# Kernel tuning notes

Hardware: AMD Instinct MI355X
Metric: run time of the kernel (lower is better)

Reference implementation:

```python
import jax, jax.numpy as jnp
import numpy as np

NUM_EMB = 10_000_000
EMB_DIM = 3
B = 16384
HIST = 50
K = 128


def setup_inputs() -> dict:
    key = jax.random.key(0)
    k1, k2, k3, k4, k5, k6, k7, k8, k9 = jax.random.split(key, 9)
    eb_input = jax.random.randint(k1, (B * HIST,), 0, NUM_EMB, dtype=jnp.int64)
    eb_offset = (jnp.arange(B, dtype=jnp.int64) * HIST)  # bag starts
    mlp_input = jax.random.normal(k2, (B, K), dtype=jnp.float32)
    # learned params
    emb_weight = jax.random.normal(k3, (NUM_EMB, EMB_DIM), dtype=jnp.float32)
    w0 = jax.random.normal(k4, (12, K), dtype=jnp.float32) * (1.0 / np.sqrt(K))
    b0 = jax.random.normal(k5, (12,), dtype=jnp.float32) * 0.01
    w1 = jax.random.normal(k6, (6, 12), dtype=jnp.float32) * (1.0 / np.sqrt(12))
    b1 = jax.random.normal(k7, (6,), dtype=jnp.float32) * 0.01
    w2 = jax.random.normal(k8, (3, 6), dtype=jnp.float32) * (1.0 / np.sqrt(6))
    b2 = jax.random.normal(k9, (3,), dtype=jnp.float32) * 0.01
    return {"eb_input": eb_input, "eb_offset": eb_offset, "mlp_input": mlp_input,
            "emb_weight": emb_weight, "w0": w0, "b0": b0, "w1": w1, "b1": b1,
            "w2": w2, "b2": b2}


def _embedding_bag_mean(weight, indices, offsets, num_bags):
    # bag id for each index position (offsets are sorted bag starts, offsets[0]=0)
    n = indices.shape[0]
    seg = jnp.searchsorted(offsets, jnp.arange(n, dtype=offsets.dtype), side='right') - 1
    rows = weight[indices]                                   # [N, 3] gather
    sums = jax.ops.segment_sum(rows, seg, num_segments=num_bags)          # [B, 3]
    cnts = jax.ops.segment_sum(jnp.ones((n,), weight.dtype), seg, num_segments=num_bags)
    return sums / jnp.maximum(cnts, 1.0)[:, None]            # mean mode; empty bag -> 0


def reference(eb_input, eb_offset, mlp_input, emb_weight, w0, b0, w1, b1, w2, b2):
    # All 3 EmbeddingBags alias the SAME module (python list * 3), so one lookup suffices.
    eb_out = _embedding_bag_mean(emb_weight, eb_input, eb_offset, mlp_input.shape[0])
    h = mlp_input @ w0.T + b0
    h = h @ w1.T + b1
    mlp_out = h @ w2.T + b2                                   # [B, 3]
    return jnp.concatenate([eb_out, eb_out, eb_out, mlp_out], axis=1)  # [B, 12]
```

## Files before the change

kernel.cpp:

```cpp
#include <hip/hip_runtime.h>


#define KDIM 128

__global__ __launch_bounds__(KDIM) void collapse_weights_kernel(
    const float* __restrict__ w0, const float* __restrict__ b0,
    const float* __restrict__ w1, const float* __restrict__ b1,
    const float* __restrict__ w2, const float* __restrict__ b2,
    float* __restrict__ ws)
{
    __shared__ float t[6][KDIM];
    __shared__ float tb[6];

    const int k = threadIdx.x;
    for (int i = 0; i < 6; ++i) {
        float acc = 0.f;
        for (int j = 0; j < 12; ++j)
            acc += w1[i * 12 + j] * w0[j * KDIM + k];
        t[i][k] = acc;
    }
    if (k < 6) {
        float acc = 0.f;
        for (int j = 0; j < 12; ++j)
            acc += w1[k * 12 + j] * b0[j];
        tb[k] = acc + b1[k];
    }
    __syncthreads();

    for (int o = 0; o < 3; ++o) {
        float acc = 0.f;
        for (int i = 0; i < 6; ++i)
            acc += w2[o * 6 + i] * t[i][k];
        ws[o * KDIM + k] = acc;
    }
    if (k == 0) {
        for (int o = 0; o < 3; ++o) {
            float acc = 0.f;
            for (int i = 0; i < 6; ++i)
                acc += w2[o * 6 + i] * tb[i];
            ws[3 * KDIM + o] = acc + b2[o];
        }
    }
}

__global__ __launch_bounds__(256) void fused_embbag_mlp_kernel(
    const int* __restrict__ eb_input,
    const int* __restrict__ eb_offset,
    const float* __restrict__ mlp_input,
    const float* __restrict__ emb_weight,
    const float* __restrict__ ws,
    float* __restrict__ out,
    int n_indices, int num_bags)
{
    const int lane = threadIdx.x & 63;
    const int wave = threadIdx.x >> 6;
    const int bag  = blockIdx.x * (blockDim.x >> 6) + wave;
    if (bag >= num_bags) return;

    const int c = lane & 3;
    const int q = lane >> 2;

    const int start = eb_offset[bag];
    const int end   = (bag + 1 < num_bags) ? eb_offset[bag + 1] : n_indices;
    const int cnt   = end - start;

    float s = 0.f;
    float m = 0.f;

    if (c < 3 && cnt > 0) {
        const int last = end - 1;
        const int p0 = start + q, p1 = p0 + 16, p2 = p1 + 16, p3 = p2 + 16;
        const int j0 = min(p0, last), j1 = min(p1, last),
                  j2 = min(p2, last), j3 = min(p3, last);
        const int i0 = eb_input[j0];
        const int i1 = eb_input[j1];
        const int i2 = eb_input[j2];
        const int i3 = eb_input[j3];
        const float g0 = emb_weight[(long long)i0 * 3 + c];
        const float g1 = emb_weight[(long long)i1 * 3 + c];
        const float g2 = emb_weight[(long long)i2 * 3 + c];
        const float g3 = emb_weight[(long long)i3 * 3 + c];
        s = (p0 < end ? g0 : 0.f) + (p1 < end ? g1 : 0.f)
          + (p2 < end ? g2 : 0.f) + (p3 < end ? g3 : 0.f);
        for (int r = start + 64 + q; r < end; r += 16)
            s += emb_weight[(long long)eb_input[r] * 3 + c];

        const float4* xp = (const float4*)(mlp_input + (long long)bag * KDIM + q * 8);
        const float4* wp = (const float4*)(ws + c * KDIM + q * 8);
        const float4 x0 = xp[0], x1 = xp[1];
        const float4 wv0 = wp[0], wv1 = wp[1];
        m = x0.x * wv0.x + x0.y * wv0.y + x0.z * wv0.z + x0.w * wv0.w
          + x1.x * wv1.x + x1.y * wv1.y + x1.z * wv1.z + x1.w * wv1.w;
    }

    #pragma unroll
    for (int off = 4; off <= 32; off <<= 1) {
        s += __shfl_xor(s, off, 64);
        m += __shfl_xor(m, off, 64);
    }

    if (c < 3 && q < 4) {
        const float inv = 1.0f / fmaxf((float)cnt, 1.0f);
        const int col = q * 3 + c;
        const float v = (q < 3) ? s * inv : (m + ws[3 * KDIM + c]);
        out[(long long)bag * 12 + col] = v;
    }
}

extern "C" void kernel_launch(void* const* d_in, const int* in_sizes, int n_in,
                              void* d_out, int out_size, void* d_ws, size_t ws_size,
                              hipStream_t stream) {
    const int*   eb_input   = (const int*)d_in[0];
    const int*   eb_offset  = (const int*)d_in[1];
    const float* mlp_input  = (const float*)d_in[2];
    const float* emb_weight = (const float*)d_in[3];
    const float* w0 = (const float*)d_in[4];
    const float* b0 = (const float*)d_in[5];
    const float* w1 = (const float*)d_in[6];
    const float* b1 = (const float*)d_in[7];
    const float* w2 = (const float*)d_in[8];
    const float* b2 = (const float*)d_in[9];
    float* out = (float*)d_out;
    float* ws  = (float*)d_ws;

    const int n_indices = in_sizes[0];
    const int num_bags  = in_sizes[1];

    collapse_weights_kernel<<<1, KDIM, 0, stream>>>(w0, b0, w1, b1, w2, b2, ws);

    const int waves_per_block = 4;
    const int grid = (num_bags + waves_per_block - 1) / waves_per_block;
    fused_embbag_mlp_kernel<<<grid, 256, 0, stream>>>(
        eb_input, eb_offset, mlp_input, emb_weight, ws, out, n_indices, num_bags);
}
```

Baseline: 197.3 us.

## Remap lanes to one index per lane with 3-float row gathers and interleaved weights

Each lane now handles one index of the bag and loads the full 3-float embedding row, where before lanes were split across channel and position slots with a quarter of them idle. The collapsed MLP weights are stored interleaved as [k][4], so each lane does the dot product for two K elements across all three outputs. The reduction grows to six shuffle-reduced values over the full wave, which adds shuffle instructions. The row gather now issues a single request per index instead of three separate per-channel loads.

New measurement: 196.8 us. About the same (-0.2%).

```diff
diff --git a/kernel.cpp b/kernel.cpp
--- a/kernel.cpp
+++ b/kernel.cpp
@@ -2,6 +2,8 @@
 
 
 #define KDIM 128
+
+struct F3 { float x, y, z; };
 
 __global__ __launch_bounds__(KDIM) void collapse_weights_kernel(
     const float* __restrict__ w0, const float* __restrict__ b0,
@@ -31,14 +33,15 @@
         float acc = 0.f;
         for (int i = 0; i < 6; ++i)
             acc += w2[o * 6 + i] * t[i][k];
-        ws[o * KDIM + k] = acc;
+        ws[k * 4 + o] = acc;
     }
+    ws[k * 4 + 3] = 0.f;
     if (k == 0) {
         for (int o = 0; o < 3; ++o) {
             float acc = 0.f;
             for (int i = 0; i < 6; ++i)
                 acc += w2[o * 6 + i] * tb[i];
-            ws[3 * KDIM + o] = acc + b2[o];
+            ws[512 + o] = acc + b2[o];
         }
     }
 }
@@ -57,53 +60,50 @@
     const int bag  = blockIdx.x * (blockDim.x >> 6) + wave;
     if (bag >= num_bags) return;
 
-    const int c = lane & 3;
-    const int q = lane >> 2;
-
     const int start = eb_offset[bag];
     const int end   = (bag + 1 < num_bags) ? eb_offset[bag + 1] : n_indices;
     const int cnt   = end - start;
 
-    float s = 0.f;
-    float m = 0.f;
+    const float2 x  = *(const float2*)(mlp_input + bag * KDIM + lane * 2);
+    const float4 t0 = *(const float4*)(ws + lane * 8);
+    const float4 t1 = *(const float4*)(ws + lane * 8 + 4);
+    float m0 = x.x * t0.x + x.y * t1.x;
+    float m1 = x.x * t0.y + x.y * t1.y;
+    float m2 = x.x * t0.z + x.y * t1.z;
 
-    if (c < 3 && cnt > 0) {
-        const int last = end - 1;
-        const int p0 = start + q, p1 = p0 + 16, p2 = p1 + 16, p3 = p2 + 16;
-        const int j0 = min(p0, last), j1 = min(p1, last),
-                  j2 = min(p2, last), j3 = min(p3, last);
-        const int i0 = eb_input[j0];
-        const int i1 = eb_input[j1];
-        const int i2 = eb_input[j2];
-        const int i3 = eb_input[j3];
-        const float g0 = emb_weight[(long long)i0 * 3 + c];
-        const float g1 = emb_weight[(long long)i1 * 3 + c];
-        const float g2 = emb_weight[(long long)i2 * 3 + c];
-        const float g3 = emb_weight[(long long)i3 * 3 + c];
-        s = (p0 < end ? g0 : 0.f) + (p1 < end ? g1 : 0.f)
-          + (p2 < end ? g2 : 0.f) + (p3 < end ? g3 : 0.f);
-        for (int r = start + 64 + q; r < end; r += 16)
-            s += emb_weight[(long long)eb_input[r] * 3 + c];
-
-        const float4* xp = (const float4*)(mlp_input + (long long)bag * KDIM + q * 8);
-        const float4* wp = (const float4*)(ws + c * KDIM + q * 8);
-        const float4 x0 = xp[0], x1 = xp[1];
-        const float4 wv0 = wp[0], wv1 = wp[1];
-        m = x0.x * wv0.x + x0.y * wv0.y + x0.z * wv0.z + x0.w * wv0.w
-          + x1.x * wv1.x + x1.y * wv1.y + x1.z * wv1.z + x1.w * wv1.w;
+    float sx = 0.f, sy = 0.f, sz = 0.f;
+    if (lane < cnt) {
+        const int idx = eb_input[start + lane];
+        const F3 r = *(const F3*)(emb_weight + idx * 3);
+        sx = r.x; sy = r.y; sz = r.z;
+        for (int p = start + lane + 64; p < end; p += 64) {
+            const int i2 = eb_input[p];
+            const F3 r2 = *(const F3*)(emb_weight + i2 * 3);
+            sx += r2.x; sy += r2.y; sz += r2.z;
+        }
     }
 
     #pragma unroll
-    for (int off = 4; off <= 32; off <<= 1) {
-        s += __shfl_xor(s, off, 64);
-        m += __shfl_xor(m, off, 64);
+    for (int off = 1; off <= 32; off <<= 1) {
+        sx += __shfl_xor(sx, off, 64);
+        sy += __shfl_xor(sy, off, 64);
+        sz += __shfl_xor(sz, off, 64);
+        m0 += __shfl_xor(m0, off, 64);
+        m1 += __shfl_xor(m1, off, 64);
+        m2 += __shfl_xor(m2, off, 64);
     }
 
-    if (c < 3 && q < 4) {
-        const float inv = 1.0f / fmaxf((float)cnt, 1.0f);
-        const int col = q * 3 + c;
-        const float v = (q < 3) ? s * inv : (m + ws[3 * KDIM + c]);
-        out[(long long)bag * 12 + col] = v;
+    if (lane < 12) {
+        float v;
+        if (lane < 9) {
+            const float inv = 1.0f / fmaxf((float)cnt, 1.0f);
+            const int cc = lane % 3;
+            v = (cc == 0 ? sx : (cc == 1 ? sy : sz)) * inv;
+        } else {
+            const int cc = lane - 9;
+            v = (cc == 0 ? m0 : (cc == 1 ? m1 : m2)) + ws[512 + cc];
+        }
+        out[bag * 12 + lane] = v;
     }
 }
 
```
